# Optimization experiments

Measured on AMD Instinct MI355X. Metric: run time of the kernel, lower is better.

Reference implementation:

```python
import jax, jax.numpy as jnp
import numpy as np

S, B, D = 2048, 2, 2048      # seq, batch, hidden  (x is [S, B, D])
H, KV, HD = 16, 4, 128        # n_head, n_kv_head, head_dim
N_REP = H // KV               # GQA repeat factor
THETA = 10000.0


def setup_inputs() -> dict:
    key = jax.random.key(0)
    ks = jax.random.split(key, 5)
    sc = 1.0 / np.sqrt(D)
    x = jax.random.normal(ks[0], (S, B, D), jnp.float32)
    Wq = jax.random.normal(ks[1], (D, H * HD), jnp.float32) * sc
    Wk = jax.random.normal(ks[2], (D, KV * HD), jnp.float32) * sc
    Wv = jax.random.normal(ks[3], (D, KV * HD), jnp.float32) * sc
    Wo = jax.random.normal(ks[4], (H * HD, D), jnp.float32) * sc
    return {"x": x, "Wq": Wq, "Wk": Wk, "Wv": Wv, "Wo": Wo}


def _rope_cos_sin(seq_len, dim, theta):
    inv_freq = 1.0 / (theta ** (jnp.arange(0, dim, 2, dtype=jnp.float32) / dim))
    t = jnp.arange(seq_len, dtype=jnp.float32)
    freqs = jnp.outer(t, inv_freq)                  # [S, dim/2]
    emb = jnp.concatenate([freqs, freqs], axis=-1)  # [S, dim]
    return jnp.cos(emb), jnp.sin(emb)


def _rotate_half(u):
    u1, u2 = jnp.split(u, 2, axis=-1)
    return jnp.concatenate([-u2, u1], axis=-1)


def reference(x, Wq, Wk, Wv, Wo):
    # projections (torch Linear without bias; W stored as [in, out] here)
    q = (x @ Wq).reshape(S, B, H, HD)
    k = (x @ Wk).reshape(S, B, KV, HD)
    v = (x @ Wv).reshape(S, B, KV, HD)

    # RoPE (full rotary, partial_rotary_factor == 1.0)
    cos, sin = _rope_cos_sin(S, HD, THETA)
    cos = cos[:, None, None, :]  # [S,1,1,HD] broadcasts over B, heads
    sin = sin[:, None, None, :]
    q = q * cos + _rotate_half(q) * sin
    k = k * cos + _rotate_half(k) * sin

    # GQA: repeat_interleave kv heads to match query heads
    k = jnp.repeat(k, N_REP, axis=2)
    v = jnp.repeat(v, N_REP, axis=2)

    # [S,B,H,HD] -> [B,H,S,HD]
    q = q.transpose(1, 2, 0, 3)
    k = k.transpose(1, 2, 0, 3)
    v = v.transpose(1, 2, 0, 3)

    # causal SDPA (dropout_p = 0 in eval)
    scale = 1.0 / np.sqrt(HD)
    scores = jnp.einsum('bhqd,bhkd->bhqk', q, k) * scale
    causal = jnp.tril(jnp.ones((S, S), dtype=bool))
    scores = jnp.where(causal, scores, jnp.finfo(scores.dtype).min)
    probs = jax.nn.softmax(scores, axis=-1)
    out = jnp.einsum('bhqk,bhkd->bhqd', probs, v)

    # [B,H,S,HD] -> [S,B,D], then output projection
    out = out.transpose(2, 0, 1, 3).reshape(S, B, D)
    return out @ Wo
```

## Files before the change

kernel.cpp:

```cpp
#include <hip/hip_runtime.h>
#include <hip/hip_bf16.h>
#include <cstdint>
#include <math.h>

#define S_LEN   2048
#define B_SZ    2
#define D_MODEL 2048
#define NH      16
#define NKV     4
#define HD      128
#define ROWS    (S_LEN * B_SZ)
#define NQKV    3072
#define SCALE   0.08838834764831845f

typedef __attribute__((ext_vector_type(8))) short short8;
typedef __attribute__((ext_vector_type(4))) float f32x4;

__device__ __forceinline__ short f2bf(float f) {
  union { float f; unsigned u; } v; v.f = f;
  unsigned r = v.u + 0x7fffu + ((v.u >> 16) & 1u);
  return (short)(r >> 16);
}
__device__ __forceinline__ float bf2f(short x) {
  union { unsigned u; float f; } v;
  v.u = ((unsigned)(unsigned short)x) << 16;
  return v.f;
}

__device__ __forceinline__ void async16(const short* g, short* l) {
  __builtin_amdgcn_global_load_lds(
      (const __attribute__((address_space(1))) void*)(uintptr_t)(const void*)g,
      (__attribute__((address_space(3))) void*)(uintptr_t)(void*)l,
      16, 0, 0);
}

__global__ void cvt_bf16_kernel(const float* __restrict__ src, short* __restrict__ dst, int n4) {
  int t = blockIdx.x * blockDim.x + threadIdx.x;
  if (t >= n4) return;
  float4 v = ((const float4*)src)[t];
  short4 o;
  o.x = f2bf(v.x); o.y = f2bf(v.y); o.z = f2bf(v.z); o.w = f2bf(v.w);
  *(short4*)(dst + (size_t)t * 4) = o;
}

__global__ void wtrans_qkv_kernel(const float* __restrict__ Wq,
                                  const float* __restrict__ Wk,
                                  const float* __restrict__ Wv,
                                  short* __restrict__ dst) {
  __shared__ float tile[32][33];
  const int bx = blockIdx.x;
  const float* src;
  int Ndim, n0, drow;
  if (bx < 64)      { src = Wq; Ndim = 2048; n0 = bx * 32;        drow = n0; }
  else if (bx < 80) { src = Wk; Ndim = 512;  n0 = (bx - 64) * 32; drow = 2048 + n0; }
  else              { src = Wv; Ndim = 512;  n0 = (bx - 80) * 32; drow = 2560 + n0; }
  const int k0 = blockIdx.y * 32;
  for (int r = threadIdx.y; r < 32; r += 8)
    tile[r][threadIdx.x] = src[(size_t)(k0 + r) * Ndim + n0 + threadIdx.x];
  __syncthreads();
  for (int r = threadIdx.y; r < 32; r += 8)
    dst[(size_t)(drow + r) * 2048 + k0 + threadIdx.x] = f2bf(tile[threadIdx.x][r]);
}

__global__ void wtrans_kernel(const float* __restrict__ src, short* __restrict__ dst,
                              int Kdim, int Ndim) {
  __shared__ float tile[32][33];
  int n0 = blockIdx.x * 32, k0 = blockIdx.y * 32;
  for (int r = threadIdx.y; r < 32; r += 8)
    tile[r][threadIdx.x] = src[(size_t)(k0 + r) * Ndim + n0 + threadIdx.x];
  __syncthreads();
  for (int r = threadIdx.y; r < 32; r += 8)
    dst[(size_t)(n0 + r) * Kdim + k0 + threadIdx.x] = f2bf(tile[threadIdx.x][r]);
}

template<int BM, int BF16OUT>
__global__ __launch_bounds__(512, 2) void gemm2_kernel(const short* __restrict__ A,
    const short* __restrict__ Bt, void* __restrict__ Cv, int N, int K) {
  constexpr int MI  = BM / 32;
  constexpr int NPH = MI / 2;
  constexpr int FA  = BM / 16;
  constexpr int FB  = 16;
  constexpr int TC  = (FA + FB) / 8;
  constexpr int ASZ = FA * 512;
  constexpr int BUFS = ASZ + FB * 512;
  __shared__ alignas(16) short lds[4 * BUFS];

  const int tid  = threadIdx.x;
  const int w    = tid >> 6, lane = tid & 63;
  const int quad = lane >> 4, lr = lane & 15;
  const int wm   = w >> 2, wn = w & 3;

  const int nwg = gridDim.x;
  const int id  = (blockIdx.x & 7) * (nwg >> 3) + (blockIdx.x >> 3);
  const int nbx = N >> 8;
  const int bx = id % nbx, by = id / nbx;
  const int m0 = by * BM, n0 = bx * 256;

  const short* gsrc[TC];
#pragma unroll
  for (int c = 0; c < TC; ++c) {
    const int ft = w * TC + c;
    const short* base = (ft < FA) ? (A  + (size_t)(m0 + ft * 16 + lr) * K)
                                  : (Bt + (size_t)(n0 + (ft - FA) * 16 + lr) * K);
    gsrc[c] = base + quad * 8;
  }

  f32x4 acc[MI][4];
#pragma unroll
  for (int i = 0; i < MI; ++i)
#pragma unroll
    for (int j = 0; j < 4; ++j) acc[i][j] = (f32x4){0.f, 0.f, 0.f, 0.f};

  auto stage = [&](int t, int c) {
    async16(gsrc[c] + t * 32, lds + (t & 3) * BUFS + (w * TC + c) * 512);
  };

  const int NT = K >> 5;
#pragma unroll
  for (int t = 0; t < 3; ++t)
#pragma unroll
    for (int c = 0; c < TC; ++c) stage(t, c);
  asm volatile("s_waitcnt vmcnt(%0)" :: "n"(2 * TC) : "memory");
  __builtin_amdgcn_s_barrier();
  asm volatile("" ::: "memory");

  for (int t = 0; t < NT; ++t) {
    const short* la = lds + (t & 3) * BUFS;
    const short* lb = la + ASZ;
    const bool pre = (t + 3) < NT;
    short8 b[4];
#pragma unroll
    for (int p = 0; p < NPH; ++p) {
      if (p == 0) {
#pragma unroll
        for (int j = 0; j < 4; ++j)
          b[j] = *(const short8*)(lb + (wn * 4 + j) * 512 + lane * 8);
      }
      short8 a0 = *(const short8*)(la + (wm * MI + 2 * p)     * 512 + lane * 8);
      short8 a1 = *(const short8*)(la + (wm * MI + 2 * p + 1) * 512 + lane * 8);
      if (pre) {
        if (p == 0) {
#pragma unroll
          for (int c = 0; c <= TC - NPH; ++c) stage(t + 3, c);
        } else {
          stage(t + 3, p + (TC - NPH));
        }
      }
      asm volatile("" ::: "memory");
      __builtin_amdgcn_s_barrier();
      asm volatile("" ::: "memory");
      __builtin_amdgcn_s_setprio(1);
#pragma unroll
      for (int j = 0; j < 4; ++j)
        acc[2 * p][j] = __builtin_amdgcn_mfma_f32_16x16x32_bf16(a0, b[j], acc[2 * p][j], 0, 0, 0);
#pragma unroll
      for (int j = 0; j < 4; ++j)
        acc[2 * p + 1][j] = __builtin_amdgcn_mfma_f32_16x16x32_bf16(a1, b[j], acc[2 * p + 1][j], 0, 0, 0);
      __builtin_amdgcn_s_setprio(0);
    }

    if (t < NT - 1) {
      if (t < NT - 3)       asm volatile("s_waitcnt vmcnt(%0)" :: "n"(2 * TC) : "memory");
      else if (t == NT - 3) asm volatile("s_waitcnt vmcnt(%0)" :: "n"(TC) : "memory");
      else                  asm volatile("s_waitcnt vmcnt(0)" ::: "memory");
      asm volatile("" ::: "memory");
      __builtin_amdgcn_s_barrier();
      asm volatile("" ::: "memory");
    }
  }

#pragma unroll
  for (int i = 0; i < MI; ++i) {
    const int row = m0 + wm * (BM / 2) + i * 16 + quad * 4;
#pragma unroll
    for (int j = 0; j < 4; ++j) {
      const int col = n0 + wn * 64 + j * 16 + lr;
#pragma unroll
      for (int r = 0; r < 4; ++r) {
        const float v = acc[i][j][r];
        if (BF16OUT) ((short*)Cv)[(size_t)(row + r) * N + col] = f2bf(v);
        else         ((float*)Cv)[(size_t)(row + r) * N + col] = v;
      }
    }
  }
}

__global__ void rope_kernel(const short* __restrict__ QKVb, short* __restrict__ Qb,
                            short* __restrict__ Kpack) {
  const int head = blockIdx.y;
  const int t = blockIdx.x * blockDim.x + threadIdx.x;
  const int i = t & 63;
  const int row = t >> 6;
  const int s = row >> 1;
  const int b = row & 1;
  float inv_freq = __expf(-(float)i * (1.0f / 64.0f) * 9.210340371976184f);
  float ang = (float)s * inv_freq;
  float sn, cs;
  __sincosf(ang, &sn, &cs);
  if (head < NH) {
    const short* p = QKVb + (size_t)row * NQKV + head * HD;
    float v1 = bf2f(p[i]), v2 = bf2f(p[i + 64]);
    short* q = Qb + ((size_t)(b * NH + head) * S_LEN + s) * HD;
    q[i]      = f2bf((v1 * cs - v2 * sn) * SCALE);
    q[i + 64] = f2bf((v2 * cs + v1 * sn) * SCALE);
  } else {
    const int kv = head - NH;
    const short* p = QKVb + (size_t)row * NQKV + NH * HD + kv * HD;
    float v1 = bf2f(p[i]), v2 = bf2f(p[i + 64]);
    float k1 = v1 * cs - v2 * sn;
    float k2 = v2 * cs + v1 * sn;
    short* kp = Kpack + (size_t)(b * NKV + kv) * S_LEN * HD;
    const int tile = s >> 4, lrr = s & 15;
    const int d1 = i, d2 = i + 64;
    kp[(size_t)((tile * 4 + (d1 >> 5)) * 64 + ((d1 >> 3) & 3) * 16 + lrr) * 8 + (d1 & 7)] = f2bf(k1);
    kp[(size_t)((tile * 4 + (d2 >> 5)) * 64 + ((d2 >> 3) & 3) * 16 + lrr) * 8 + (d2 & 7)] = f2bf(k2);
  }
}

__global__ void vpack_kernel(const short* __restrict__ QKVb, short* __restrict__ Vpack) {
  __shared__ short tile[32][136];
  const int tid = threadIdx.x;
  const int chunk = blockIdx.x & 63, stream = blockIdx.x >> 6;
  const int b = stream >> 2, kv = stream & 3;
  const int vcol = NH * HD + NKV * HD + kv * HD;
  {
    const int r = tid >> 3, c = (tid & 7) * 16;
    const short* src = QKVb + (size_t)((chunk * 32 + r) * B_SZ + b) * NQKV + vcol + c;
    *(short8*)(&tile[r][c])     = *(const short8*)(src);
    *(short8*)(&tile[r][c + 8]) = *(const short8*)(src + 8);
  }
  __syncthreads();
  const int wave = tid >> 6, lane = tid & 63, quad = lane >> 4, lr = lane & 15;
  short* dst = Vpack + (size_t)stream * HD * S_LEN + chunk * 4096 + lane * 8;
#pragma unroll
  for (int k = 0; k < 2; ++k) {
    const int dt = wave + k * 4;
    short8 v;
#pragma unroll
    for (int j = 0; j < 8; ++j) v[j] = tile[quad * 8 + j][dt * 16 + lr];
    *(short8*)(dst + dt * 512) = v;
  }
}

#define PSP 72

template<bool MASK>
__device__ __forceinline__ void attn_iter64(
    const short* __restrict__ Ks, const short* __restrict__ Vs,
    short* __restrict__ Psw, const short8 qf[4], int kv0, int nt, int qlim,
    int quad, int lr, int lane, f32x4 o[8], float& m_i, float& l_i)
{
  const int lane_off = lane * 8;
  f32x4 sc[4];
#pragma unroll
  for (int t = 0; t < 4; ++t) {
    if (t < nt) {
      const short* kp = Ks + t * 2048 + lane_off;
      f32x4 s = (f32x4){0.f, 0.f, 0.f, 0.f};
#pragma unroll
      for (int c = 0; c < 4; ++c) {
        short8 kf = *(const short8*)(kp + c * 512);
        s = __builtin_amdgcn_mfma_f32_16x16x32_bf16(kf, qf[c], s, 0, 0, 0);
      }
      sc[t] = s;
    } else {
      sc[t] = (f32x4){-3.0e38f, -3.0e38f, -3.0e38f, -3.0e38f};
    }
  }
  if (MASK) {
#pragma unroll
    for (int t = 0; t < 4; ++t)
#pragma unroll
      for (int r = 0; r < 4; ++r)
        if (kv0 + t * 16 + quad * 4 + r > qlim) sc[t][r] = -3.0e38f;
  }
  float mb = -3.0e38f;
#pragma unroll
  for (int t = 0; t < 4; ++t)
#pragma unroll
    for (int r = 0; r < 4; ++r) mb = fmaxf(mb, sc[t][r]);
  mb = fmaxf(mb, __shfl_xor(mb, 16, 64));
  mb = fmaxf(mb, __shfl_xor(mb, 32, 64));
  const float mnew = fmaxf(m_i, mb);
  const float alpha = __expf(m_i - mnew);
  m_i = mnew;
  float rs = 0.f;
#pragma unroll
  for (int t = 0; t < 4; ++t) {
    float p0 = __expf(sc[t][0] - mnew);
    float p1 = __expf(sc[t][1] - mnew);
    float p2 = __expf(sc[t][2] - mnew);
    float p3 = __expf(sc[t][3] - mnew);
    rs += (p0 + p1) + (p2 + p3);
    __hip_bfloat162 pk01 = __float22bfloat162_rn(make_float2(p0, p1));
    __hip_bfloat162 pk23 = __float22bfloat162_rn(make_float2(p2, p3));
    __hip_bfloat162* pd = (__hip_bfloat162*)(Psw + lr * PSP + t * 16 + quad * 4);
    pd[0] = pk01;
    pd[1] = pk23;
  }
  rs += __shfl_xor(rs, 16, 64);
  rs += __shfl_xor(rs, 32, 64);
  l_i = l_i * alpha + rs;
#pragma unroll
  for (int n = 0; n < 8; ++n)
#pragma unroll
    for (int r = 0; r < 4; ++r) o[n][r] *= alpha;
  short8 pb0 = *(const short8*)(Psw + lr * PSP + quad * 8);
#pragma unroll
  for (int dt = 0; dt < 8; ++dt) {
    short8 vf = *(const short8*)(Vs + dt * 512 + lane_off);
    o[dt] = __builtin_amdgcn_mfma_f32_16x16x32_bf16(vf, pb0, o[dt], 0, 0, 0);
  }
  if (!MASK || nt > 2) {
    short8 pb1 = *(const short8*)(Psw + lr * PSP + 32 + quad * 8);
#pragma unroll
    for (int dt = 0; dt < 8; ++dt) {
      short8 vf = *(const short8*)(Vs + 4096 + dt * 512 + lane_off);
      o[dt] = __builtin_amdgcn_mfma_f32_16x16x32_bf16(vf, pb1, o[dt], 0, 0, 0);
    }
  }
}

__global__ __launch_bounds__(256) void attn_kernel(const short* __restrict__ Qb,
    const short* __restrict__ Kpack, const short* __restrict__ Vpack,
    short* __restrict__ Ob) {
  __shared__ alignas(16) short Ks[64 * HD];
  __shared__ alignas(16) short Vs[64 * HD];
  __shared__ alignas(16) short Ps[4][16 * PSP];
  const int tid = threadIdx.x, wave = tid >> 6, lane = tid & 63;
  const int quad = lane >> 4, lr = lane & 15;
  const int bid = blockIdx.x;
  const int sid  = bid & 7;
  const int hsub = (bid >> 3) & 3;
  const int qg   = 31 - (bid >> 5);
  const int b = sid >> 2, kvh = sid & 3;
  const int h = kvh * 4 + hsub;
  const int qw = (qg * 4 + wave) * 16;

  const short* Qp  = Qb    + ((size_t)(b * NH + h) * S_LEN + qw) * HD;
  const short* Kpk = Kpack + (size_t)(b * NKV + kvh) * S_LEN * HD;
  const short* Vpk = Vpack + (size_t)(b * NKV + kvh) * HD * S_LEN;
  short* Psw = &Ps[wave][0];

  short8 qf[4];
#pragma unroll
  for (int c = 0; c < 4; ++c)
    qf[c] = *(const short8*)(Qp + lr * HD + c * 32 + quad * 8);

  f32x4 o[8];
#pragma unroll
  for (int n = 0; n < 8; ++n) o[n] = (f32x4){0.f, 0.f, 0.f, 0.f};
  float m_i = -3.0e38f, l_i = 0.f;

  const int qlim = qw + lr;
  for (int it = 0; it <= qg; ++it) {
    const int kv0 = it * 64;
    __syncthreads();
    {
      const short* gk = Kpk + (size_t)kv0 * HD;
      const short* gv = Vpk + (size_t)(kv0 >> 5) * 4096;
#pragma unroll
      for (int k = 0; k < 4; ++k) {
        const int off = (wave * 4 + k) * 512;
        async16(gk + off + lane * 8, Ks + off);
        async16(gv + off + lane * 8, Vs + off);
      }
    }
    __syncthreads();
    if (it < qg)
      attn_iter64<false>(Ks, Vs, Psw, qf, kv0, 4, qlim, quad, lr, lane, o, m_i, l_i);
    else
      attn_iter64<true>(Ks, Vs, Psw, qf, kv0, wave + 1, qlim, quad, lr, lane, o, m_i, l_i);
  }

  const float invl = 1.0f / l_i;
  short* op = Ob + ((size_t)(qw + lr) * B_SZ + b) * D_MODEL + h * HD + quad * 4;
#pragma unroll
  for (int dt = 0; dt < 8; ++dt) {
    short4 ov;
    ov.x = f2bf(o[dt][0] * invl);
    ov.y = f2bf(o[dt][1] * invl);
    ov.z = f2bf(o[dt][2] * invl);
    ov.w = f2bf(o[dt][3] * invl);
    *(short4*)(op + dt * 16) = ov;
  }
}

extern "C" void kernel_launch(void* const* d_in, const int* in_sizes, int n_in,
                              void* d_out, int out_size, void* d_ws, size_t ws_size,
                              hipStream_t stream) {
  (void)in_sizes; (void)n_in; (void)out_size; (void)ws_size;
  const float* x  = (const float*)d_in[0];
  const float* Wq = (const float*)d_in[1];
  const float* Wk = (const float*)d_in[2];
  const float* Wv = (const float*)d_in[3];
  const float* Wo = (const float*)d_in[4];
  float* out = (float*)d_out;
  char* ws = (char*)d_ws;

  short* Wqkv_t = (short*)(ws);
  short* xb     = (short*)(ws + 12582912);
  short* Qb     = (short*)(ws);
  short* Kpack  = (short*)(ws + 16777216);
  short* Vpack  = (short*)(ws + 25165824);
  short* QKVb   = (short*)(ws + 29360128);
  short* Ob     = (short*)(ws + 29360128);
  short* Wo_t   = (short*)(ws + 54525952);

  dim3 tblk(32, 8);

  cvt_bf16_kernel<<<(ROWS * D_MODEL / 4 + 255) / 256, 256, 0, stream>>>(x, xb, ROWS * D_MODEL / 4);
  wtrans_qkv_kernel<<<dim3(96, 64), tblk, 0, stream>>>(Wq, Wk, Wv, Wqkv_t);
  wtrans_kernel<<<dim3(64, 64), tblk, 0, stream>>>(Wo, Wo_t, 2048, 2048);
  gemm2_kernel<256, 1><<<dim3((NQKV / 256) * (ROWS / 256)), 512, 0, stream>>>(xb, Wqkv_t, QKVb, NQKV, D_MODEL);
  rope_kernel<<<dim3(1024, NH + NKV), 256, 0, stream>>>(QKVb, Qb, Kpack);
  vpack_kernel<<<dim3(512), 256, 0, stream>>>(QKVb, Vpack);
  attn_kernel<<<dim3(1024), 256, 0, stream>>>(Qb, Kpack, Vpack, Ob);
  gemm2_kernel<128, 0><<<dim3((D_MODEL / 256) * (ROWS / 128)), 512, 0, stream>>>(Ob, Wo_t, out, D_MODEL, D_MODEL);
}
```

Baseline: 318.4 us.

## Double-buffer K/V tiles in attention and move GEMM to K=64 double-buffered stages

```diff
diff --git a/kernel.cpp b/kernel.cpp
--- a/kernel.cpp
+++ b/kernel.cpp
@@ -32,6 +32,10 @@
       (const __attribute__((address_space(1))) void*)(uintptr_t)(const void*)g,
       (__attribute__((address_space(3))) void*)(uintptr_t)(void*)l,
       16, 0, 0);
+}
+
+template<int N> __device__ __forceinline__ void vm_wait() {
+  asm volatile("s_waitcnt vmcnt(%0)" :: "n"(N) : "memory");
 }
 
 __global__ void cvt_bf16_kernel(const float* __restrict__ src, short* __restrict__ dst, int n4) {
@@ -74,16 +78,17 @@
 }
 
 template<int BM, int BF16OUT>
-__global__ __launch_bounds__(512, 2) void gemm2_kernel(const short* __restrict__ A,
+__global__ __launch_bounds__(512, 2) void gemm3_kernel(const short* __restrict__ A,
     const short* __restrict__ Bt, void* __restrict__ Cv, int N, int K) {
-  constexpr int MI  = BM / 32;
-  constexpr int NPH = MI / 2;
-  constexpr int FA  = BM / 16;
-  constexpr int FB  = 16;
-  constexpr int TC  = (FA + FB) / 8;
-  constexpr int ASZ = FA * 512;
-  constexpr int BUFS = ASZ + FB * 512;
-  __shared__ alignas(16) short lds[4 * BUFS];
+  constexpr int MGRP  = BM / 16;
+  constexpr int MI    = BM / 32;
+  constexpr int NP    = MI / 2;
+  constexpr int BCALLS = 4;
+  constexpr int ACALLS = MGRP / 4;
+  constexpr int CALLS = BCALLS + ACALLS;
+  constexpr int BS_SH = 16384;
+  constexpr int BUFSH = BS_SH + MGRP * 1024;
+  __shared__ alignas(16) short lds[2 * BUFSH];
 
   const int tid  = threadIdx.x;
   const int w    = tid >> 6, lane = tid & 63;
@@ -96,13 +101,20 @@
   const int bx = id % nbx, by = id / nbx;
   const int m0 = by * BM, n0 = bx * 256;
 
-  const short* gsrc[TC];
-#pragma unroll
-  for (int c = 0; c < TC; ++c) {
-    const int ft = w * TC + c;
-    const short* base = (ft < FA) ? (A  + (size_t)(m0 + ft * 16 + lr) * K)
-                                  : (Bt + (size_t)(n0 + (ft - FA) * 16 + lr) * K);
-    gsrc[c] = base + quad * 8;
+  const short* gsrc[CALLS];
+  int dsts[CALLS];
+#pragma unroll
+  for (int c = 0; c < CALLS; ++c) {
+    if (c < BCALLS) {
+      const int sb = c * 8 + w, ng = sb >> 1, kk = sb & 1;
+      gsrc[c] = Bt + (size_t)(n0 + ng * 16 + lr) * K + kk * 32 + quad * 8;
+      dsts[c] = sb * 512;
+    } else {
+      const int p = c - BCALLS;
+      const int mg = (w >> 2) * (MGRP / 2) + 2 * p + ((w >> 1) & 1), kk = w & 1;
+      gsrc[c] = A + (size_t)(m0 + mg * 16 + lr) * K + kk * 32 + quad * 8;
+      dsts[c] = BS_SH + (p * 8 + w) * 512;
+    }
   }
 
   f32x4 acc[MI][4];
@@ -112,57 +124,66 @@
     for (int j = 0; j < 4; ++j) acc[i][j] = (f32x4){0.f, 0.f, 0.f, 0.f};
 
   auto stage = [&](int t, int c) {
-    async16(gsrc[c] + t * 32, lds + (t & 3) * BUFS + (w * TC + c) * 512);
+    async16(gsrc[c] + (size_t)t * 64, lds + (t & 1) * BUFSH + dsts[c]);
   };
 
-  const int NT = K >> 5;
-#pragma unroll
-  for (int t = 0; t < 3; ++t)
-#pragma unroll
-    for (int c = 0; c < TC; ++c) stage(t, c);
-  asm volatile("s_waitcnt vmcnt(%0)" :: "n"(2 * TC) : "memory");
+  const int NT = K >> 6;
+#pragma unroll
+  for (int c = 0; c < CALLS; ++c) stage(0, c);
+  if (BM == 256) vm_wait<3>(); else vm_wait<1>();
   __builtin_amdgcn_s_barrier();
   asm volatile("" ::: "memory");
 
   for (int t = 0; t < NT; ++t) {
-    const short* la = lds + (t & 3) * BUFS;
-    const short* lb = la + ASZ;
-    const bool pre = (t + 3) < NT;
-    short8 b[4];
-#pragma unroll
-    for (int p = 0; p < NPH; ++p) {
+    const short* lb = lds + (t & 1) * BUFSH;
+    const bool pre = (t + 1) < NT;
+    short8 b[4][2];
+#pragma unroll
+    for (int p = 0; p < NP; ++p) {
       if (p == 0) {
 #pragma unroll
         for (int j = 0; j < 4; ++j)
-          b[j] = *(const short8*)(lb + (wn * 4 + j) * 512 + lane * 8);
+#pragma unroll
+          for (int kk = 0; kk < 2; ++kk)
+            b[j][kk] = *(const short8*)(lb + ((wn * 4 + j) * 2 + kk) * 512 + lane * 8);
       }
-      short8 a0 = *(const short8*)(la + (wm * MI + 2 * p)     * 512 + lane * 8);
-      short8 a1 = *(const short8*)(la + (wm * MI + 2 * p + 1) * 512 + lane * 8);
+      short8 a[2][2];
+#pragma unroll
+      for (int e = 0; e < 2; ++e)
+#pragma unroll
+        for (int kk = 0; kk < 2; ++kk)
+          a[e][kk] = *(const short8*)(lb + BS_SH + (p * 8 + (wm * 2 + e) * 2 + kk) * 512 + lane * 8);
       if (pre) {
-        if (p == 0) {
-#pragma unroll
-          for (int c = 0; c <= TC - NPH; ++c) stage(t + 3, c);
-        } else {
-          stage(t + 3, p + (TC - NPH));
-        }
+        if (NP == 4) { stage(t + 1, 2 * p); stage(t + 1, 2 * p + 1); }
+        else         { stage(t + 1, 3 * p); stage(t + 1, 3 * p + 1); stage(t + 1, 3 * p + 2); }
       }
       asm volatile("" ::: "memory");
       __builtin_amdgcn_s_barrier();
-      asm volatile("" ::: "memory");
+      asm volatile("s_waitcnt lgkmcnt(0)" ::: "memory");
       __builtin_amdgcn_s_setprio(1);
 #pragma unroll
-      for (int j = 0; j < 4; ++j)
-        acc[2 * p][j] = __builtin_amdgcn_mfma_f32_16x16x32_bf16(a0, b[j], acc[2 * p][j], 0, 0, 0);
-#pragma unroll
-      for (int j = 0; j < 4; ++j)
-        acc[2 * p + 1][j] = __builtin_amdgcn_mfma_f32_16x16x32_bf16(a1, b[j], acc[2 * p + 1][j], 0, 0, 0);
+      for (int kk = 0; kk < 2; ++kk)
+#pragma unroll
+        for (int e = 0; e < 2; ++e)
+#pragma unroll
+          for (int j = 0; j < 4; ++j)
+            acc[2 * p + e][j] = __builtin_amdgcn_mfma_f32_16x16x32_bf16(a[e][kk], b[j][kk], acc[2 * p + e][j], 0, 0, 0);
       __builtin_amdgcn_s_setprio(0);
-    }
-
-    if (t < NT - 1) {
-      if (t < NT - 3)       asm volatile("s_waitcnt vmcnt(%0)" :: "n"(2 * TC) : "memory");
-      else if (t == NT - 3) asm volatile("s_waitcnt vmcnt(%0)" :: "n"(TC) : "memory");
-      else                  asm volatile("s_waitcnt vmcnt(0)" ::: "memory");
+      if (pre) {
+        if (NP == 4) {
+          if (p == 0) vm_wait<4>(); else if (p == 1) vm_wait<5>();
+          else if (p == 2) vm_wait<6>(); else vm_wait<3>();
+        } else {
+          if (p == 0) vm_wait<3>(); else vm_wait<1>();
+        }
+      } else {
+        if (NP == 4) {
+          if (p == 0) vm_wait<2>(); else if (p == 1) vm_wait<1>();
+          else if (p == 2) vm_wait<0>();
+        } else {
+          if (p == 0) vm_wait<0>();
+        }
+      }
       asm volatile("" ::: "memory");
       __builtin_amdgcn_s_barrier();
       asm volatile("" ::: "memory");
@@ -324,8 +345,8 @@
 __global__ __launch_bounds__(256) void attn_kernel(const short* __restrict__ Qb,
     const short* __restrict__ Kpack, const short* __restrict__ Vpack,
     short* __restrict__ Ob) {
-  __shared__ alignas(16) short Ks[64 * HD];
-  __shared__ alignas(16) short Vs[64 * HD];
+  __shared__ alignas(16) short Ks[2][64 * HD];
+  __shared__ alignas(16) short Vs[2][64 * HD];
   __shared__ alignas(16) short Ps[4][16 * PSP];
   const int tid = threadIdx.x, wave = tid >> 6, lane = tid & 63;
   const int quad = lane >> 4, lr = lane & 15;
@@ -352,25 +373,29 @@
   for (int n = 0; n < 8; ++n) o[n] = (f32x4){0.f, 0.f, 0.f, 0.f};
   float m_i = -3.0e38f, l_i = 0.f;
 
+  auto stage_kv = [&](int it) {
+    const int buf = it & 1;
+    const int kv0 = it * 64;
+    const short* gk = Kpk + (size_t)kv0 * HD;
+    const short* gv = Vpk + (size_t)(kv0 >> 5) * 4096;
+#pragma unroll
+    for (int k = 0; k < 4; ++k) {
+      const int off = (wave * 4 + k) * 512;
+      async16(gk + off + lane * 8, &Ks[buf][off]);
+      async16(gv + off + lane * 8, &Vs[buf][off]);
+    }
+  };
+
   const int qlim = qw + lr;
+  stage_kv(0);
   for (int it = 0; it <= qg; ++it) {
-    const int kv0 = it * 64;
     __syncthreads();
-    {
-      const short* gk = Kpk + (size_t)kv0 * HD;
-      const short* gv = Vpk + (size_t)(kv0 >> 5) * 4096;
-#pragma unroll
-      for (int k = 0; k < 4; ++k) {
-        const int off = (wave * 4 + k) * 512;
-        async16(gk + off + lane * 8, Ks + off);
-        async16(gv + off + lane * 8, Vs + off);
-      }
-    }
-    __syncthreads();
+    if (it < qg) stage_kv(it + 1);
+    const int buf = it & 1;
     if (it < qg)
-      attn_iter64<false>(Ks, Vs, Psw, qf, kv0, 4, qlim, quad, lr, lane, o, m_i, l_i);
+      attn_iter64<false>(Ks[buf], Vs[buf], Psw, qf, it * 64, 4, qlim, quad, lr, lane, o, m_i, l_i);
     else
-      attn_iter64<true>(Ks, Vs, Psw, qf, kv0, wave + 1, qlim, quad, lr, lane, o, m_i, l_i);
+      attn_iter64<true>(Ks[buf], Vs[buf], Psw, qf, it * 64, wave + 1, qlim, quad, lr, lane, o, m_i, l_i);
   }
 
   const float invl = 1.0f / l_i;
@@ -412,9 +437,9 @@
   cvt_bf16_kernel<<<(ROWS * D_MODEL / 4 + 255) / 256, 256, 0, stream>>>(x, xb, ROWS * D_MODEL / 4);
   wtrans_qkv_kernel<<<dim3(96, 64), tblk, 0, stream>>>(Wq, Wk, Wv, Wqkv_t);
   wtrans_kernel<<<dim3(64, 64), tblk, 0, stream>>>(Wo, Wo_t, 2048, 2048);
-  gemm2_kernel<256, 1><<<dim3((NQKV / 256) * (ROWS / 256)), 512, 0, stream>>>(xb, Wqkv_t, QKVb, NQKV, D_MODEL);
+  gemm3_kernel<256, 1><<<dim3((NQKV / 256) * (ROWS / 256)), 512, 0, stream>>>(xb, Wqkv_t, QKVb, NQKV, D_MODEL);
   rope_kernel<<<dim3(1024, NH + NKV), 256, 0, stream>>>(QKVb, Qb, Kpack);
   vpack_kernel<<<dim3(512), 256, 0, stream>>>(QKVb, Vpack);
   attn_kernel<<<dim3(1024), 256, 0, stream>>>(Qb, Kpack, Vpack, Ob);
-  gemm2_kernel<128, 0><<<dim3((D_MODEL / 256) * (ROWS / 128)), 512, 0, stream>>>(Ob, Wo_t, out, D_MODEL, D_MODEL);
-}
+  gemm3_kernel<128, 0><<<dim3((D_MODEL / 256) * (ROWS / 128)), 512, 0, stream>>>(Ob, Wo_t, out, D_MODEL, D_MODEL);
+}
```

Result: slower. 338.2 us (+6.2%).
